# Kernel tuning notes

Measured on AMD Instinct MI355X. Metric: run time of the kernel, lower is better.

Reference implementation:

```python
import jax, jax.numpy as jnp
import numpy as np

HEADS = 16
DIM_HEAD = 64
SCALE = DIM_HEAD ** -0.5


def shift(x):
    # Transformer-XL relative shift trick. x: [..., i, j] -> [..., i, j]
    *pre, i, j = x.shape
    x = jnp.concatenate([x, jnp.zeros((*pre, i, i), x.dtype)], axis=-1)
    l = i + j - 1
    x = x.reshape(*pre, -1)
    pad = (-x.shape[-1]) % l
    x = jnp.concatenate([x, jnp.zeros((*pre, pad), x.dtype)], axis=-1)
    x = x.reshape(*pre, -1, l)
    return x[..., :i, i - 1:]


def setup_inputs() -> dict:
    key = jax.random.key(0)
    ks = jax.random.split(key, 8)
    b, t, e = 2, 1024, 1024
    mem_len, lmem_len = 1024, 128
    kv_len = t + mem_len + lmem_len
    return {
        "x": jax.random.normal(ks[0], (b, t, e), jnp.float32),
        "mem": jax.random.normal(ks[1], (b, mem_len, e), jnp.float32),
        "lmem": jax.random.normal(ks[2], (b, lmem_len, e), jnp.float32),
        "pos_emb": jax.random.normal(ks[3], (HEADS, kv_len, DIM_HEAD), jnp.float32),
        "input_mask": jnp.ones((b, t), bool),
        "Wq": jax.random.normal(ks[4], (e, e), jnp.float32) * 0.02,
        "Wkv": jax.random.normal(ks[5], (e, 2 * e), jnp.float32) * 0.02,
        "Wout": jax.random.normal(ks[6], (e, e), jnp.float32) * 0.02,
        "bout": jnp.zeros((e,), jnp.float32),
    }


def reference(x, mem, lmem, pos_emb, input_mask, Wq, Wkv, Wout, bout):
    b, t, e = x.shape
    h, dh = HEADS, DIM_HEAD
    mem_len, lmem_len = mem.shape[1], lmem.shape[1]
    total_mem = mem_len + lmem_len

    q = x @ Wq
    kv_input = jnp.concatenate([lmem, mem, x], axis=1)  # [b, kv_len, e]
    kv_len = kv_input.shape[1]
    k, v = jnp.split(kv_input @ Wkv, 2, axis=-1)

    def merge_heads(z):
        return z.reshape(b, -1, h, dh).transpose(0, 2, 1, 3)  # [b, h, n, dh]

    q, k, v = merge_heads(q), merge_heads(k), merge_heads(v)

    dots = jnp.einsum('bhid,bhjd->bhij', q, k) * SCALE  # [b, h, t, kv_len]

    pe = pos_emb[:, -kv_len:].astype(q.dtype)
    pos_dots = jnp.einsum('bhid,hjd->bhij', q, pe) * SCALE
    dots = dots + shift(pos_dots)

    mask_value = -jnp.finfo(dots.dtype).max

    pad_mask = input_mask[:, None, :, None] & input_mask[:, None, None, :]
    pad_mask = jnp.pad(pad_mask, ((0, 0), (0, 0), (0, 0), (total_mem, 0)), constant_values=True)
    dots = jnp.where(pad_mask, dots, mask_value)

    causal = jnp.triu(jnp.ones((t, t + total_mem), bool), k=1 + total_mem)
    dots = jnp.where(causal[None, None], mask_value, dots)

    attn = jax.nn.softmax(dots, axis=-1)
    out = jnp.einsum('bhij,bhjd->bhid', attn, v)
    out = out.transpose(0, 2, 1, 3).reshape(b, t, -1)
    return out @ Wout + bout
```

## Files before the change

kernel.cpp:

```cpp
#include <hip/hip_runtime.h>


typedef unsigned int   u32;
typedef unsigned short u16;
typedef unsigned long long u64;
typedef __attribute__((ext_vector_type(8))) short short8;
typedef __attribute__((ext_vector_type(4))) float f32x4;
typedef __attribute__((ext_vector_type(4))) u32   u32x4;

#define DEVI static __device__ __forceinline__
#define MFMA_BF16 __builtin_amdgcn_mfma_f32_16x16x32_bf16

DEVI u16 f2bf(float f) {
  u32 u = __builtin_bit_cast(u32, f);
  return (u16)((u + 0x7FFFu + ((u >> 16) & 1u)) >> 16);
}
DEVI float bf2f(u16 h) { u32 u = (u32)h << 16; return __builtin_bit_cast(float, u); }
DEVI u32 pk2(float lo, float hi) { return (u32)f2bf(lo) | ((u32)f2bf(hi) << 16); }

constexpr int T_ = 1024, E_ = 1024, KV = 2176, H_ = 16;

__global__ void k_prep_kvin(const float* __restrict__ x, const float* __restrict__ mem,
                            const float* __restrict__ lmem, u16* __restrict__ kvin) {
  int u = blockIdx.x * 256 + threadIdx.x;
  int b = u / (KV * E_ / 8);
  int r = u % (KV * E_ / 8);
  int j = r >> 7;
  int e8 = (r & 127) << 3;
  const float* src;
  if (j < 128)        src = lmem + ((size_t)(b * 128 + j) * E_ + e8);
  else if (j < 1152)  src = mem  + ((size_t)(b * 1024 + (j - 128)) * E_ + e8);
  else                src = x    + ((size_t)(b * 1024 + (j - 1152)) * E_ + e8);
  float4 a = ((const float4*)src)[0];
  float4 c = ((const float4*)src)[1];
  u32x4 o = { pk2(a.x, a.y), pk2(a.z, a.w), pk2(c.x, c.y), pk2(c.z, c.w) };
  *(u32x4*)(kvin + (size_t)u * 8) = o;
}

__global__ void k_prep_pe(const float* __restrict__ pos, u16* __restrict__ pe) {
  size_t u = (size_t)blockIdx.x * 256 + threadIdx.x;
  float4 a = ((const float4*)(pos + u * 8))[0];
  float4 c = ((const float4*)(pos + u * 8))[1];
  u32x4 o = { pk2(a.x, a.y), pk2(a.z, a.w), pk2(c.x, c.y), pk2(c.z, c.w) };
  *(u32x4*)(pe + u * 8) = o;
}

__global__ void k_transp(const float* __restrict__ src, u16* __restrict__ dst, int K, int N) {
  __shared__ float tile[32][33];
  int n0 = blockIdx.x * 32, k0 = blockIdx.y * 32;
  int tx = threadIdx.x, ty = threadIdx.y;
#pragma unroll
  for (int s = 0; s < 4; s++) tile[ty + 8 * s][tx] = src[(size_t)(k0 + ty + 8 * s) * N + n0 + tx];
  __syncthreads();
#pragma unroll
  for (int s = 0; s < 4; s++)
    dst[(size_t)(n0 + ty + 8 * s) * K + k0 + tx] = f2bf(tile[tx][ty + 8 * s]);
}

__global__ __launch_bounds__(256, 2)
void k_gemm_qkv(const u16* __restrict__ kvin, const u16* __restrict__ WallT,
                u16* __restrict__ qb, u16* __restrict__ kb, u16* __restrict__ vtb) {
  int bid = blockIdx.x;
  int b = bid / 336;
  int r = bid % 336;
  int nt, mt;
  if (r < 64) { nt = r >> 3; mt = 9 + (r & 7); }
  else { r -= 64; nt = 8 + r / 17; mt = r % 17; }

  const u16* A  = kvin + ((size_t)b * KV + (size_t)mt * 128) * E_;
  const u16* Bm = WallT + (size_t)nt * 128 * E_;

  __shared__ u16 As[128 * 40];
  __shared__ u16 Bs[128 * 40];

  int t = threadIdx.x;
  int wid = t >> 6, lane = t & 63;
  int wr = wid >> 1, wc = wid & 1;
  int l15 = lane & 15, l4 = lane >> 4;

  f32x4 acc[4][4] = {};
  int arow = t >> 2, aslot = t & 3;

  u32x4 ra[2], rb[2];
#pragma unroll
  for (int p = 0; p < 2; p++) {
    ra[p] = *(const u32x4*)(A  + (size_t)(arow + 64 * p) * E_ + aslot * 8);
    rb[p] = *(const u32x4*)(Bm + (size_t)(arow + 64 * p) * E_ + aslot * 8);
  }
  for (int kt = 0; kt < 32; kt++) {
    __syncthreads();
#pragma unroll
    for (int p = 0; p < 2; p++) {
      *(u32x4*)(As + (arow + 64 * p) * 40 + aslot * 8) = ra[p];
      *(u32x4*)(Bs + (arow + 64 * p) * 40 + aslot * 8) = rb[p];
    }
    __syncthreads();
    if (kt + 1 < 32) {
      int k0 = (kt + 1) * 32;
#pragma unroll
      for (int p = 0; p < 2; p++) {
        ra[p] = *(const u32x4*)(A  + (size_t)(arow + 64 * p) * E_ + k0 + aslot * 8);
        rb[p] = *(const u32x4*)(Bm + (size_t)(arow + 64 * p) * E_ + k0 + aslot * 8);
      }
    }
    short8 af[4], bfv[4];
#pragma unroll
    for (int m = 0; m < 4; m++)
      af[m] = *(const short8*)(As + (wr * 64 + m * 16 + l15) * 40 + l4 * 8);
#pragma unroll
    for (int n = 0; n < 4; n++)
      bfv[n] = *(const short8*)(Bs + (wc * 64 + n * 16 + l15) * 40 + l4 * 8);
#pragma unroll
    for (int m = 0; m < 4; m++)
#pragma unroll
      for (int n = 0; n < 4; n++)
        acc[m][n] = MFMA_BF16(af[m], bfv[n], acc[m][n], 0, 0, 0);
  }
  int grow_base = mt * 128 + wr * 64;
  int ncol_base = nt * 128 + wc * 64;
  if (nt < 8) {
#pragma unroll
    for (int m = 0; m < 4; m++)
#pragma unroll
      for (int n = 0; n < 4; n++) {
        int col = ncol_base + n * 16 + l15;
        int head = col >> 6, d = col & 63;
#pragma unroll
        for (int rg = 0; rg < 4; rg++) {
          int row = grow_base + m * 16 + l4 * 4 + rg - 1152;
          qb[(((size_t)b * 16 + head) * 1024 + row) * 64 + d] = f2bf(acc[m][n][rg] * 0.125f);
        }
      }
  } else if (nt < 16) {
#pragma unroll
    for (int m = 0; m < 4; m++)
#pragma unroll
      for (int n = 0; n < 4; n++) {
        int c = ncol_base + n * 16 + l15 - 1024;
        int head = c >> 6, d = c & 63;
#pragma unroll
        for (int rg = 0; rg < 4; rg++) {
          int row = grow_base + m * 16 + l4 * 4 + rg;
          kb[(((size_t)b * 16 + head) * KV + row) * 64 + d] = f2bf(acc[m][n][rg]);
        }
      }
  } else {
#pragma unroll
    for (int m = 0; m < 4; m++)
#pragma unroll
      for (int n = 0; n < 4; n++) {
        int c = ncol_base + n * 16 + l15 - 2048;
        int head = c >> 6, d = c & 63;
        int jb = grow_base + m * 16 + l4 * 4;
        u64 pv = (u64)f2bf(acc[m][n][0]) | ((u64)f2bf(acc[m][n][1]) << 16)
               | ((u64)f2bf(acc[m][n][2]) << 32) | ((u64)f2bf(acc[m][n][3]) << 48);
        *(u64*)(vtb + (((size_t)b * 16 + head) * 64 + d) * KV + jb) = pv;
      }
  }
}

__global__ __launch_bounds__(256, 2)
void k_attn(const u16* __restrict__ qb, const u16* __restrict__ kb,
            const u16* __restrict__ vtb, const u16* __restrict__ peb,
            u16* __restrict__ ao) {
  int bid = blockIdx.x;
  int xcd = bid & 7, bk = bid >> 3;
  int it = bk & 15, g = bk >> 4;
  int bh = g * 8 + xcd;
  int b = bh >> 4, h = bh & 15;
  int i0 = it * 64;

  __shared__ u16 Klds[64][72];
  __shared__ u16 Vt[64][72];
  __shared__ u16 PEs[64][72];
  __shared__ u16 Band[64][136];
  __shared__ u16 Pb[4][16][72];

  int t = threadIdx.x, wid = t >> 6, lane = t & 63;
  int l15 = lane & 15, l4 = lane >> 4;
  int il = wid * 16 + l15;
  int srow = t >> 3, ssl = t & 7;

  const u16* kbase  = kb  + (size_t)bh * KV * 64;
  const u16* vtbase = vtb + (size_t)bh * 64 * KV;
  const u16* pebase = peb + (size_t)h * KV * 64;

  const u16* qptr = qb + ((size_t)bh * 1024 + i0 + il) * 64 + l4 * 8;
  short8 qf0 = *(const short8*)qptr;
  short8 qf1 = *(const short8*)(qptr + 32);

  auto band_step = [&](int prb) {
#pragma unroll
    for (int rc = 0; rc < 4; rc++) {
      f32x4 a = {};
      short8 p0 = *(const short8*)(&PEs[rc * 16 + l15][l4 * 8]);
      short8 p1 = *(const short8*)(&PEs[rc * 16 + l15][32 + l4 * 8]);
      a = MFMA_BF16(p0, qf0, a, 0, 0, 0);
      a = MFMA_BF16(p1, qf1, a, 0, 0, 0);
      int cb = prb + rc * 16 + l4 * 4;
#pragma unroll
      for (int rg = 0; rg < 4; rg++)
        Band[il][(cb + rg) & 127] = f2bf(a[rg]);
    }
  };

  {
    int pr0 = 960 - i0;
    u32x4 d0 = *(const u32x4*)(pebase + (size_t)(pr0 + srow) * 64 + ssl * 8);
    u32x4 d1 = *(const u32x4*)(pebase + (size_t)(pr0 + srow + 32) * 64 + ssl * 8);
    *(u32x4*)(&PEs[srow][ssl * 8]) = d0;
    *(u32x4*)(&PEs[srow + 32][ssl * 8]) = d1;
    __syncthreads();
    band_step(pr0);
  }

  f32x4 Of[4] = {};
  float mr = -1e30f, lr = 0.f;
  int njt = it + 19;

  u32x4 rk0, rk1, rv0, rv1, rp0, rp1;
  auto load_regs = [&](int jt_) {
    int j0_ = jt_ * 64;
    rk0 = *(const u32x4*)(kbase + (size_t)(j0_ + srow) * 64 + ssl * 8);
    rk1 = *(const u32x4*)(kbase + (size_t)(j0_ + srow + 32) * 64 + ssl * 8);
    rv0 = *(const u32x4*)(vtbase + (size_t)srow * KV + j0_ + ssl * 8);
    rv1 = *(const u32x4*)(vtbase + (size_t)(srow + 32) * KV + j0_ + ssl * 8);
    int pb = 1024 + j0_ - i0;
    int p0 = pb + srow;      p0 = p0 > 2175 ? 2175 : p0;
    int p1 = pb + srow + 32; p1 = p1 > 2175 ? 2175 : p1;
    rp0 = *(const u32x4*)(pebase + (size_t)p0 * 64 + ssl * 8);
    rp1 = *(const u32x4*)(pebase + (size_t)p1 * 64 + ssl * 8);
  };
  load_regs(0);

  for (int jt = 0; jt < njt; jt++) {
    bool domask = (jt == njt - 1);

    __syncthreads();
    *(u32x4*)(&Klds[srow][ssl * 8]) = rk0;
    *(u32x4*)(&Klds[srow + 32][ssl * 8]) = rk1;
    *(u32x4*)(&Vt[srow][ssl * 8]) = rv0;
    *(u32x4*)(&Vt[srow + 32][ssl * 8]) = rv1;
    *(u32x4*)(&PEs[srow][ssl * 8]) = rp0;
    *(u32x4*)(&PEs[srow + 32][ssl * 8]) = rp1;
    __syncthreads();
    if (jt + 1 < njt) load_regs(jt + 1);

    f32x4 sc[4];
#pragma unroll
    for (int jc = 0; jc < 4; jc++) {
      f32x4 a = {};
      short8 k0 = *(const short8*)(&Klds[jc * 16 + l15][l4 * 8]);
      short8 k1 = *(const short8*)(&Klds[jc * 16 + l15][32 + l4 * 8]);
      a = MFMA_BF16(k0, qf0, a, 0, 0, 0);
      a = MFMA_BF16(k1, qf1, a, 0, 0, 0);
      sc[jc] = a;
    }
    band_step(1024 + 64 * jt - i0);
    __syncthreads();

    float P[4][4];
    float mx = -1e30f;
    int bbase = 1023 + 64 * jt - i0 - il;
#pragma unroll
    for (int jc = 0; jc < 4; jc++)
#pragma unroll
      for (int rg = 0; rg < 4; rg++) {
        int jj = jc * 16 + l4 * 4 + rg;
        float v = sc[jc][rg] + bf2f(Band[il][(bbase + jj) & 127]);
        if (domask && (jj > il)) v = -1e30f;
        P[jc][rg] = v;
        mx = fmaxf(mx, v);
      }
    mx = fmaxf(mx, __shfl_xor(mx, 16, 64));
    mx = fmaxf(mx, __shfl_xor(mx, 32, 64));
    float mnew = fmaxf(mr, mx);
    float fac = __expf(mr - mnew);
    mr = mnew;
    float ps = 0.f;
#pragma unroll
    for (int jc = 0; jc < 4; jc++)
#pragma unroll
      for (int rg = 0; rg < 4; rg++) {
        float p = __expf(P[jc][rg] - mnew);
        P[jc][rg] = p;
        ps += p;
      }
    ps += __shfl_xor(ps, 16, 64);
    ps += __shfl_xor(ps, 32, 64);
    lr = lr * fac + ps;
#pragma unroll
    for (int dc = 0; dc < 4; dc++) Of[dc] *= fac;

#pragma unroll
    for (int jc = 0; jc < 4; jc++)
#pragma unroll
      for (int rg = 0; rg < 4; rg++)
        Pb[wid][l15][jc * 16 + l4 * 4 + rg] = f2bf(P[jc][rg]);
    __syncthreads();

    short8 pB0 = *(const short8*)(&Pb[wid][l15][l4 * 8]);
    short8 pB1 = *(const short8*)(&Pb[wid][l15][32 + l4 * 8]);
#pragma unroll
    for (int df = 0; df < 4; df++) {
      short8 v0 = *(const short8*)(&Vt[df * 16 + l15][l4 * 8]);
      short8 v1 = *(const short8*)(&Vt[df * 16 + l15][32 + l4 * 8]);
      Of[df] = MFMA_BF16(v0, pB0, Of[df], 0, 0, 0);
      Of[df] = MFMA_BF16(v1, pB1, Of[df], 0, 0, 0);
    }
  }

  float inv = 1.0f / lr;
  size_t ob = ((size_t)b * 1024 + i0 + il) * 1024 + h * 64;
#pragma unroll
  for (int df = 0; df < 4; df++) {
    u64 pv = (u64)f2bf(Of[df][0] * inv)         | ((u64)f2bf(Of[df][1] * inv) << 16)
           | ((u64)f2bf(Of[df][2] * inv) << 32) | ((u64)f2bf(Of[df][3] * inv) << 48);
    *(u64*)(ao + ob + df * 16 + l4 * 4) = pv;
  }
}

__global__ __launch_bounds__(256, 2)
void k_gemm_out(const u16* __restrict__ ao, const u16* __restrict__ WoT,
                const float* __restrict__ bias, float* __restrict__ out) {
  int mt = blockIdx.x & 31, nt = blockIdx.x >> 5;
  const u16* A  = ao  + (size_t)mt * 64 * E_;
  const u16* Bm = WoT + (size_t)nt * 128 * E_;
  __shared__ u16 As[64 * 40];
  __shared__ u16 Bs[128 * 40];
  int t = threadIdx.x, wid = t >> 6, lane = t & 63;
  int wr = wid >> 1, wc = wid & 1, l15 = lane & 15, l4 = lane >> 4;
  f32x4 acc[2][4] = {};
  int arow = t >> 2, aslot = t & 3;

  u32x4 ra, rb[2];
  ra = *(const u32x4*)(A + (size_t)arow * E_ + aslot * 8);
#pragma unroll
  for (int p = 0; p < 2; p++)
    rb[p] = *(const u32x4*)(Bm + (size_t)(arow + 64 * p) * E_ + aslot * 8);
  for (int kt = 0; kt < 32; kt++) {
    __syncthreads();
    *(u32x4*)(As + arow * 40 + aslot * 8) = ra;
#pragma unroll
    for (int p = 0; p < 2; p++)
      *(u32x4*)(Bs + (arow + 64 * p) * 40 + aslot * 8) = rb[p];
    __syncthreads();
    if (kt + 1 < 32) {
      int k0 = (kt + 1) * 32;
      ra = *(const u32x4*)(A + (size_t)arow * E_ + k0 + aslot * 8);
#pragma unroll
      for (int p = 0; p < 2; p++)
        rb[p] = *(const u32x4*)(Bm + (size_t)(arow + 64 * p) * E_ + k0 + aslot * 8);
    }
    short8 af[2], bfv[4];
#pragma unroll
    for (int m = 0; m < 2; m++)
      af[m] = *(const short8*)(As + (wr * 32 + m * 16 + l15) * 40 + l4 * 8);
#pragma unroll
    for (int n = 0; n < 4; n++)
      bfv[n] = *(const short8*)(Bs + (wc * 64 + n * 16 + l15) * 40 + l4 * 8);
#pragma unroll
    for (int m = 0; m < 2; m++)
#pragma unroll
      for (int n = 0; n < 4; n++)
        acc[m][n] = MFMA_BF16(af[m], bfv[n], acc[m][n], 0, 0, 0);
  }
#pragma unroll
  for (int n = 0; n < 4; n++) {
    int col = nt * 128 + wc * 64 + n * 16 + l15;
    float bv = bias[col];
#pragma unroll
    for (int m = 0; m < 2; m++) {
      int row = mt * 64 + wr * 32 + m * 16 + l4 * 4;
#pragma unroll
      for (int rg = 0; rg < 4; rg++)
        out[(size_t)(row + rg) * E_ + col] = acc[m][n][rg] + bv;
    }
  }
}

extern "C" void kernel_launch(void* const* d_in, const int* in_sizes, int n_in,
                              void* d_out, int out_size, void* d_ws, size_t ws_size,
                              hipStream_t stream) {
  (void)in_sizes; (void)n_in; (void)out_size; (void)ws_size;
  const float* x    = (const float*)d_in[0];
  const float* mem  = (const float*)d_in[1];
  const float* lmem = (const float*)d_in[2];
  const float* pos  = (const float*)d_in[3];
  const float* Wq   = (const float*)d_in[5];
  const float* Wkv  = (const float*)d_in[6];
  const float* Wout = (const float*)d_in[7];
  const float* bout = (const float*)d_in[8];
  float* out = (float*)d_out;

  u16* kvin  = (u16*)d_ws;
  u16* pe    = kvin  + (size_t)2 * KV * E_;
  u16* WallT = pe    + (size_t)H_ * KV * 64;
  u16* WoT   = WallT + (size_t)3072 * E_;
  u16* qb    = WoT   + (size_t)E_ * E_;
  u16* kb    = qb    + (size_t)2 * H_ * T_ * 64;
  u16* vtb   = kb    + (size_t)2 * H_ * KV * 64;
  u16* ao    = vtb   + (size_t)2 * H_ * KV * 64;

  k_prep_kvin<<<2176, 256, 0, stream>>>(x, mem, lmem, kvin);
  k_prep_pe<<<1088, 256, 0, stream>>>(pos, pe);
  k_transp<<<dim3(32, 32), dim3(32, 8), 0, stream>>>(Wq,   WallT,             1024, 1024);
  k_transp<<<dim3(64, 32), dim3(32, 8), 0, stream>>>(Wkv,  WallT + 1024*1024, 1024, 2048);
  k_transp<<<dim3(32, 32), dim3(32, 8), 0, stream>>>(Wout, WoT,               1024, 1024);
  k_gemm_qkv<<<672, 256, 0, stream>>>(kvin, WallT, qb, kb, vtb);
  k_attn<<<512, 256, 0, stream>>>(qb, kb, vtb, pe, ao);
  k_gemm_out<<<256, 256, 0, stream>>>(ao, WoT, bout, out);
}
```

Before: 156.5 us.

## Split attention into single-wave blocks loading K/V/PE directly into registers

The attention kernel changes from 256-thread blocks covering 64 query rows to 64-thread single-wave blocks, each covering 16 rows, with four times as many blocks. K, V and positional-embedding tiles are read straight from global memory into registers instead of being staged in shared memory, which removes every __syncthreads in the loop. MFMA sections are bracketed with s_setprio. In exchange, each wave now fetches full K/V/PE tiles on its own, so global/L2 traffic rises up to fourfold, and the register-prefetch pipelining of the next tile is gone.

```diff
diff --git a/kernel.cpp b/kernel.cpp
--- a/kernel.cpp
+++ b/kernel.cpp
@@ -159,27 +159,23 @@
   }
 }
 
-__global__ __launch_bounds__(256, 2)
+__global__ __launch_bounds__(64, 2)
 void k_attn(const u16* __restrict__ qb, const u16* __restrict__ kb,
             const u16* __restrict__ vtb, const u16* __restrict__ peb,
             u16* __restrict__ ao) {
   int bid = blockIdx.x;
   int xcd = bid & 7, bk = bid >> 3;
-  int it = bk & 15, g = bk >> 4;
+  int wq = bk & 3, it = (bk >> 2) & 15, g = bk >> 6;
   int bh = g * 8 + xcd;
   int b = bh >> 4, h = bh & 15;
   int i0 = it * 64;
 
-  __shared__ u16 Klds[64][72];
-  __shared__ u16 Vt[64][72];
-  __shared__ u16 PEs[64][72];
-  __shared__ u16 Band[64][136];
-  __shared__ u16 Pb[4][16][72];
-
-  int t = threadIdx.x, wid = t >> 6, lane = t & 63;
+  __shared__ __align__(16) u16 Band[16][140];
+  __shared__ __align__(16) u16 Pb[16][72];
+
+  int lane = threadIdx.x & 63;
   int l15 = lane & 15, l4 = lane >> 4;
-  int il = wid * 16 + l15;
-  int srow = t >> 3, ssl = t & 7;
+  int il = wq * 16 + l15;
 
   const u16* kbase  = kb  + (size_t)bh * KV * 64;
   const u16* vtbase = vtb + (size_t)bh * 64 * KV;
@@ -190,88 +186,88 @@
   short8 qf1 = *(const short8*)(qptr + 32);
 
   auto band_step = [&](int prb) {
+    short8 pf[8];
+#pragma unroll
+    for (int rc = 0; rc < 4; rc++) {
+      int rr = prb + rc * 16 + l15; rr = rr > 2175 ? 2175 : rr;
+#pragma unroll
+      for (int kk = 0; kk < 2; kk++)
+        pf[rc * 2 + kk] = *(const short8*)(pebase + (size_t)rr * 64 + kk * 32 + l4 * 8);
+    }
+    f32x4 acc[4];
+    __builtin_amdgcn_s_setprio(1);
 #pragma unroll
     for (int rc = 0; rc < 4; rc++) {
       f32x4 a = {};
-      short8 p0 = *(const short8*)(&PEs[rc * 16 + l15][l4 * 8]);
-      short8 p1 = *(const short8*)(&PEs[rc * 16 + l15][32 + l4 * 8]);
-      a = MFMA_BF16(p0, qf0, a, 0, 0, 0);
-      a = MFMA_BF16(p1, qf1, a, 0, 0, 0);
-      int cb = prb + rc * 16 + l4 * 4;
+      a = MFMA_BF16(pf[rc * 2 + 0], qf0, a, 0, 0, 0);
+      a = MFMA_BF16(pf[rc * 2 + 1], qf1, a, 0, 0, 0);
+      acc[rc] = a;
+    }
+    __builtin_amdgcn_s_setprio(0);
+#pragma unroll
+    for (int rc = 0; rc < 4; rc++) {
+      int rb = prb + rc * 16 + l4 * 4 + il + 1;
 #pragma unroll
       for (int rg = 0; rg < 4; rg++)
-        Band[il][(cb + rg) & 127] = f2bf(a[rg]);
+        Band[l15][(rb + rg) & 127] = f2bf(acc[rc][rg]);
     }
   };
 
-  {
-    int pr0 = 960 - i0;
-    u32x4 d0 = *(const u32x4*)(pebase + (size_t)(pr0 + srow) * 64 + ssl * 8);
-    u32x4 d1 = *(const u32x4*)(pebase + (size_t)(pr0 + srow + 32) * 64 + ssl * 8);
-    *(u32x4*)(&PEs[srow][ssl * 8]) = d0;
-    *(u32x4*)(&PEs[srow + 32][ssl * 8]) = d1;
-    __syncthreads();
-    band_step(pr0);
-  }
+  band_step(960 - i0);
 
   f32x4 Of[4] = {};
   float mr = -1e30f, lr = 0.f;
   int njt = it + 19;
 
-  u32x4 rk0, rk1, rv0, rv1, rp0, rp1;
-  auto load_regs = [&](int jt_) {
-    int j0_ = jt_ * 64;
-    rk0 = *(const u32x4*)(kbase + (size_t)(j0_ + srow) * 64 + ssl * 8);
-    rk1 = *(const u32x4*)(kbase + (size_t)(j0_ + srow + 32) * 64 + ssl * 8);
-    rv0 = *(const u32x4*)(vtbase + (size_t)srow * KV + j0_ + ssl * 8);
-    rv1 = *(const u32x4*)(vtbase + (size_t)(srow + 32) * KV + j0_ + ssl * 8);
-    int pb = 1024 + j0_ - i0;
-    int p0 = pb + srow;      p0 = p0 > 2175 ? 2175 : p0;
-    int p1 = pb + srow + 32; p1 = p1 > 2175 ? 2175 : p1;
-    rp0 = *(const u32x4*)(pebase + (size_t)p0 * 64 + ssl * 8);
-    rp1 = *(const u32x4*)(pebase + (size_t)p1 * 64 + ssl * 8);
-  };
-  load_regs(0);
-
   for (int jt = 0; jt < njt; jt++) {
+    int j0 = jt * 64;
     bool domask = (jt == njt - 1);
 
-    __syncthreads();
-    *(u32x4*)(&Klds[srow][ssl * 8]) = rk0;
-    *(u32x4*)(&Klds[srow + 32][ssl * 8]) = rk1;
-    *(u32x4*)(&Vt[srow][ssl * 8]) = rv0;
-    *(u32x4*)(&Vt[srow + 32][ssl * 8]) = rv1;
-    *(u32x4*)(&PEs[srow][ssl * 8]) = rp0;
-    *(u32x4*)(&PEs[srow + 32][ssl * 8]) = rp1;
-    __syncthreads();
-    if (jt + 1 < njt) load_regs(jt + 1);
+    short8 kf[8];
+#pragma unroll
+    for (int jc = 0; jc < 4; jc++)
+#pragma unroll
+      for (int kk = 0; kk < 2; kk++)
+        kf[jc * 2 + kk] = *(const short8*)(kbase + (size_t)(j0 + jc * 16 + l15) * 64 + kk * 32 + l4 * 8);
 
     f32x4 sc[4];
+    __builtin_amdgcn_s_setprio(1);
 #pragma unroll
     for (int jc = 0; jc < 4; jc++) {
       f32x4 a = {};
-      short8 k0 = *(const short8*)(&Klds[jc * 16 + l15][l4 * 8]);
-      short8 k1 = *(const short8*)(&Klds[jc * 16 + l15][32 + l4 * 8]);
-      a = MFMA_BF16(k0, qf0, a, 0, 0, 0);
-      a = MFMA_BF16(k1, qf1, a, 0, 0, 0);
+      a = MFMA_BF16(kf[jc * 2 + 0], qf0, a, 0, 0, 0);
+      a = MFMA_BF16(kf[jc * 2 + 1], qf1, a, 0, 0, 0);
       sc[jc] = a;
     }
-    band_step(1024 + 64 * jt - i0);
-    __syncthreads();
+    __builtin_amdgcn_s_setprio(0);
+
+    band_step(1024 + j0 - i0);
+
+    short8 vf[8];
+#pragma unroll
+    for (int df = 0; df < 4; df++)
+#pragma unroll
+      for (int kk = 0; kk < 2; kk++)
+        vf[df * 2 + kk] = *(const short8*)(vtbase + (size_t)(df * 16 + l15) * KV + j0 + kk * 32 + l4 * 8);
+
+    asm volatile("s_waitcnt lgkmcnt(0)" ::: "memory");
+    __builtin_amdgcn_sched_barrier(0);
 
     float P[4][4];
     float mx = -1e30f;
-    int bbase = 1023 + 64 * jt - i0 - il;
-#pragma unroll
-    for (int jc = 0; jc < 4; jc++)
+    int cb0 = ((jt - it) & 1) << 6;
+#pragma unroll
+    for (int jc = 0; jc < 4; jc++) {
+      u64 bl = *(const u64*)(&Band[l15][cb0 + jc * 16 + l4 * 4]);
 #pragma unroll
       for (int rg = 0; rg < 4; rg++) {
         int jj = jc * 16 + l4 * 4 + rg;
-        float v = sc[jc][rg] + bf2f(Band[il][(bbase + jj) & 127]);
+        float v = sc[jc][rg] + bf2f((u16)(bl >> (16 * rg)));
         if (domask && (jj > il)) v = -1e30f;
         P[jc][rg] = v;
         mx = fmaxf(mx, v);
       }
+    }
     mx = fmaxf(mx, __shfl_xor(mx, 16, 64));
     mx = fmaxf(mx, __shfl_xor(mx, 32, 64));
     float mnew = fmaxf(mr, mx);
@@ -296,18 +292,20 @@
     for (int jc = 0; jc < 4; jc++)
 #pragma unroll
       for (int rg = 0; rg < 4; rg++)
-        Pb[wid][l15][jc * 16 + l4 * 4 + rg] = f2bf(P[jc][rg]);
-    __syncthreads();
-
-    short8 pB0 = *(const short8*)(&Pb[wid][l15][l4 * 8]);
-    short8 pB1 = *(const short8*)(&Pb[wid][l15][32 + l4 * 8]);
+        Pb[l15][jc * 16 + l4 * 4 + rg] = f2bf(P[jc][rg]);
+
+    asm volatile("s_waitcnt lgkmcnt(0)" ::: "memory");
+    __builtin_amdgcn_sched_barrier(0);
+
+    short8 pB0 = *(const short8*)(&Pb[l15][l4 * 8]);
+    short8 pB1 = *(const short8*)(&Pb[l15][32 + l4 * 8]);
+    __builtin_amdgcn_s_setprio(1);
 #pragma unroll
     for (int df = 0; df < 4; df++) {
-      short8 v0 = *(const short8*)(&Vt[df * 16 + l15][l4 * 8]);
-      short8 v1 = *(const short8*)(&Vt[df * 16 + l15][32 + l4 * 8]);
-      Of[df] = MFMA_BF16(v0, pB0, Of[df], 0, 0, 0);
-      Of[df] = MFMA_BF16(v1, pB1, Of[df], 0, 0, 0);
-    }
+      Of[df] = MFMA_BF16(vf[df * 2 + 0], pB0, Of[df], 0, 0, 0);
+      Of[df] = MFMA_BF16(vf[df * 2 + 1], pB1, Of[df], 0, 0, 0);
+    }
+    __builtin_amdgcn_s_setprio(0);
   }
 
   float inv = 1.0f / lr;
@@ -408,6 +406,6 @@
   k_transp<<<dim3(64, 32), dim3(32, 8), 0, stream>>>(Wkv,  WallT + 1024*1024, 1024, 2048);
   k_transp<<<dim3(32, 32), dim3(32, 8), 0, stream>>>(Wout, WoT,               1024, 1024);
   k_gemm_qkv<<<672, 256, 0, stream>>>(kvin, WallT, qb, kb, vtb);
-  k_attn<<<512, 256, 0, stream>>>(qb, kb, vtb, pe, ao);
+  k_attn<<<2048, 64, 0, stream>>>(qb, kb, vtb, pe, ao);
   k_gemm_out<<<256, 256, 0, stream>>>(ao, WoT, bout, out);
 }
```

Measured after the change: 237.6 us. +51.8%, slower.
